# Optimization experiments

Hardware: AMD Instinct MI355X
Metric: run time of the kernel (lower is better)

## Reference

```python
import jax, jax.numpy as jnp
import numpy as np

B, S, D = 8, 2048, 1024


def setup_inputs() -> dict:
    key = jax.random.key(0)
    ks = jax.random.split(key, 9)
    s = 1.0 / np.sqrt(D)
    return {
        "x": jax.random.normal(ks[0], (B, S, D), dtype=jnp.float32),
        "Wq": jax.random.normal(ks[1], (D, D), dtype=jnp.float32) * s,
        "bq": jnp.zeros((D,), dtype=jnp.float32),
        "Wk": jax.random.normal(ks[2], (D, D), dtype=jnp.float32) * s,
        "bk": jnp.zeros((D,), dtype=jnp.float32),
        "Wv": jax.random.normal(ks[3], (D, D), dtype=jnp.float32) * s,
        "bv": jnp.zeros((D,), dtype=jnp.float32),
        "Wo": jax.random.normal(ks[4], (D, D), dtype=jnp.float32) * s,
        "bo": jnp.zeros((D,), dtype=jnp.float32),
    }


def reference(x, Wq, bq, Wk, bk, Wv, bv, Wo, bo):
    # Single-head self-attention with full NxN scores (as in the torch module).
    q = jnp.einsum("bsd,de->bse", x, Wq) + bq
    k = jnp.einsum("bsd,de->bse", x, Wk) + bk
    v = jnp.einsum("bsd,de->bse", x, Wv) + bv
    scores = jnp.einsum("bqd,bkd->bqk", q, k) / jnp.sqrt(jnp.float32(D))
    attn = jax.nn.softmax(scores, axis=-1)
    y = jnp.einsum("bqk,bkd->bqd", attn, v)
    return jnp.einsum("bsd,de->bse", y, Wo) + bo
```

## Files before the change

### kernel.cpp

```cpp
#include <hip/hip_runtime.h>
#include <stdint.h>


using u16 = unsigned short;
using u32 = unsigned int;
using short8  = __attribute__((ext_vector_type(8))) short;
using floatx4 = __attribute__((ext_vector_type(4))) float;

#define GPTR(p) ((__attribute__((address_space(1))) u32*)(p))
#define LPTR(p) ((__attribute__((address_space(3))) u32*)(p))

__device__ __forceinline__ void async_cp16(const void* g, void* l) {
  __builtin_amdgcn_global_load_lds(GPTR(g), LPTR(l), 16, 0, 0);
}

__device__ __forceinline__ u16 f2bf(float f) {
  u32 u = __builtin_bit_cast(u32, f);
  u = (u + 0x7fffu + ((u >> 16) & 1u)) >> 16;
  return (u16)u;
}
__device__ __forceinline__ float bf2f(u16 h) {
  u32 u = ((u32)h) << 16;
  return __builtin_bit_cast(float, u);
}

__device__ __forceinline__ void swz(int gx, int gy, int& bx, int& by) {
  int s = blockIdx.x + gx * blockIdx.y;
  int q = s >> 3;
  by = (s & 7) * (gy >> 3) + q / gx;
  bx = q % gx;
}

__device__ __forceinline__ void gemm_core(
    const u16* __restrict__ A, const u16* __restrict__ B,
    int lda, int ldb, int K, u16* lA, u16* lB, floatx4 acc[4][4])
{
  const int tid  = threadIdx.x;
  const int lane = tid & 63;
  const int w    = tid >> 6;
  const int r8   = lane >> 3;
  const int cg   = (lane & 7) ^ r8;
  const int frow = lane & 15;
  const int fq   = lane >> 4;
  const int wrow = (w >> 1) * 64;
  const int wcol = (w & 1) * 64;

  const u16* gaL = A + (size_t)(w * 32 + r8) * lda + cg * 8;
  const u16* gbL = B + (size_t)(w * 32 + r8) * ldb + cg * 8;
  u16* lAw = lA + (w * 32) * 64;
  u16* lBw = lB + (w * 32) * 64;
  const int x0 = ((0 + fq) ^ (frow & 7)) * 8;
  const int x1 = ((4 + fq) ^ (frow & 7)) * 8;

  for (int k0 = 0; k0 < K; k0 += 64) {
    const u16* ga = gaL + k0;
    const u16* gb = gbL + k0;
#pragma unroll
    for (int t = 0; t < 4; ++t) {
      async_cp16(ga + (size_t)(t * 8) * lda, lAw + t * 8 * 64);
      async_cp16(gb + (size_t)(t * 8) * ldb, lBw + t * 8 * 64);
    }
    __syncthreads();

#pragma unroll
    for (int sub = 0; sub < 2; ++sub) {
      const int xs = sub ? x1 : x0;
      short8 af[4], bfr[4];
#pragma unroll
      for (int i = 0; i < 4; ++i)
        af[i] = *(const short8*)(lA + (wrow + i * 16 + frow) * 64 + xs);
#pragma unroll
      for (int j = 0; j < 4; ++j)
        bfr[j] = *(const short8*)(lB + (wcol + j * 16 + frow) * 64 + xs);
#pragma unroll
      for (int i = 0; i < 4; ++i)
#pragma unroll
        for (int j = 0; j < 4; ++j)
          acc[i][j] = __builtin_amdgcn_mfma_f32_16x16x32_bf16(af[i], bfr[j], acc[i][j], 0, 0, 0);
    }
    __syncthreads();
  }
}

__global__ __launch_bounds__(256) void k_cast_x(const float* __restrict__ x, u16* __restrict__ xb) {
  size_t i = ((size_t)blockIdx.x * 256 + threadIdx.x) * 8;
  float4 a = *(const float4*)(x + i);
  float4 b = *(const float4*)(x + i + 4);
  u16 o[8] __attribute__((aligned(16)));
  o[0] = f2bf(a.x); o[1] = f2bf(a.y); o[2] = f2bf(a.z); o[3] = f2bf(a.w);
  o[4] = f2bf(b.x); o[5] = f2bf(b.y); o[6] = f2bf(b.z); o[7] = f2bf(b.w);
  *(uint4*)(xb + i) = *(const uint4*)o;
}

__global__ __launch_bounds__(256) void k_cast_wt(
    const float* __restrict__ Wq, const float* __restrict__ Wk,
    const float* __restrict__ Wo, const float* __restrict__ Wv,
    u16* __restrict__ WT, u16* __restrict__ Wvb)
{
  __shared__ float t[32][33];
  const int z = blockIdx.z;
  const int c = threadIdx.x & 31, r = threadIdx.x >> 5;
  if (z == 3) {
#pragma unroll
    for (int p = 0; p < 4; ++p) {
      const size_t idx = (size_t)(blockIdx.y * 32 + r + 8 * p) * 1024 + blockIdx.x * 32 + c;
      Wvb[idx] = f2bf(Wv[idx]);
    }
    return;
  }
  const float* W = (z == 0) ? Wq : (z == 1) ? Wk : Wo;
  u16* out = WT + (size_t)z * 1024 * 1024;
#pragma unroll
  for (int p = 0; p < 4; ++p)
    t[r + 8 * p][c] = W[(size_t)(blockIdx.y * 32 + r + 8 * p) * 1024 + blockIdx.x * 32 + c];
  __syncthreads();
#pragma unroll
  for (int p = 0; p < 4; ++p)
    out[(size_t)(blockIdx.x * 32 + r + 8 * p) * 1024 + blockIdx.y * 32 + c] = f2bf(t[c][r + 8 * p]);
}

__global__ __launch_bounds__(256) void k_bvo(
    const float* __restrict__ bv, const float* __restrict__ Wo, float* __restrict__ bvo)
{
  const int nb = blockIdx.x & 3, jc = blockIdx.x >> 2;
  const int n = nb * 256 + threadIdx.x;
  float s = 0.f;
#pragma unroll 4
  for (int j = jc * 64; j < jc * 64 + 64; ++j) s += bv[j] * Wo[(size_t)j * 1024 + n];
  atomicAdd(&bvo[n], s);
}

__global__ __launch_bounds__(256, 4) void k_wvo_part(
    const u16* __restrict__ WoT, const u16* __restrict__ Wvb, float* __restrict__ Pf)
{
  __shared__ u16 lA[8192], lB[8192];
  const int bx = blockIdx.x, by = blockIdx.y, z = blockIdx.z;
  const u16* Am = WoT + (size_t)by * 128 * 1024 + z * 256;
  const u16* Bm = Wvb + (size_t)bx * 128 * 1024 + z * 256;
  floatx4 acc[4][4] = {};
  gemm_core(Am, Bm, 1024, 1024, 256, lA, lB, acc);

  float* out = Pf + (size_t)z * 1024 * 1024;
  const int lane = threadIdx.x & 63, w = threadIdx.x >> 6;
  const int wrow = (w >> 1) * 64, wcol = (w & 1) * 64;
#pragma unroll
  for (int j = 0; j < 4; ++j) {
    const int c = bx * 128 + wcol + j * 16 + (lane & 15);
#pragma unroll
    for (int i = 0; i < 4; ++i) {
      const int m0 = by * 128 + wrow + i * 16 + (lane >> 4) * 4;
#pragma unroll
      for (int r = 0; r < 4; ++r)
        out[(size_t)(m0 + r) * 1024 + c] = acc[i][j][r];
    }
  }
}

__global__ __launch_bounds__(256) void k_wvo_red(
    const float* __restrict__ Pf, u16* __restrict__ WvoT)
{
  const size_t e = ((size_t)blockIdx.x * 256 + threadIdx.x) * 8;
  u16 o[8] __attribute__((aligned(16)));
#pragma unroll
  for (int h = 0; h < 2; ++h) {
    float4 s = *(const float4*)(Pf + e + h * 4);
#pragma unroll
    for (int z = 1; z < 4; ++z) {
      float4 p = *(const float4*)(Pf + (size_t)z * 1024 * 1024 + e + h * 4);
      s.x += p.x; s.y += p.y; s.z += p.z; s.w += p.w;
    }
    o[h * 4 + 0] = f2bf(s.x); o[h * 4 + 1] = f2bf(s.y);
    o[h * 4 + 2] = f2bf(s.z); o[h * 4 + 3] = f2bf(s.w);
  }
  *(uint4*)(WvoT + e) = *(const uint4*)o;
}

__global__ __launch_bounds__(256, 4) void k_qkv(
    const u16* __restrict__ XB, const u16* __restrict__ WT,
    const float* __restrict__ bq, const float* __restrict__ bk, const float* __restrict__ bvo,
    u16* __restrict__ Q, u16* __restrict__ Kb, u16* __restrict__ Vt)
{
  __shared__ u16 smem[17408];
  u16* lA = smem;
  u16* lB = smem + 8192;
  int bx, by; swz(8, 128, bx, by);
  const int mode = blockIdx.z;
  const u16* Am = XB + (size_t)by * 128 * 1024;
  const int ws_idx = (mode == 2) ? 3 : mode;
  const u16* Bm = WT + (size_t)ws_idx * 1024 * 1024 + (size_t)bx * 128 * 1024;
  const float* bias = (mode == 0) ? bq : (mode == 1) ? bk : bvo;
  floatx4 acc[4][4] = {};
  gemm_core(Am, Bm, 1024, 1024, 1024, lA, lB, acc);

  const int tid = threadIdx.x, lane = tid & 63, w = tid >> 6;
  const int lane15 = lane & 15, fq = lane >> 4;
  const int wrow = (w >> 1) * 64, wcol = (w & 1) * 64;

  if (mode == 2) {
    u16* T = smem;
    __syncthreads();
#pragma unroll
    for (int j = 0; j < 4; ++j) {
      const int c = wcol + j * 16 + lane15;
      const float bb = bias[bx * 128 + c];
#pragma unroll
      for (int i = 0; i < 4; ++i)
#pragma unroll
        for (int r = 0; r < 4; ++r)
          T[c * 136 + wrow + i * 16 + fq * 4 + r] = f2bf(acc[i][j][r] + bb);
    }
    __syncthreads();
    const int b = by >> 4, s0 = (by & 15) * 128, c0 = bx * 128;
#pragma unroll
    for (int kk = 0; kk < 8; ++kk) {
      const int cr = (tid >> 4) + 16 * kk, pos = tid & 15;
      uint4 val = *(const uint4*)(T + cr * 136 + pos * 8);
      *(uint4*)(Vt + ((size_t)(b * 1024 + c0 + cr)) * 2048 + s0 + pos * 8) = val;
    }
    return;
  }

#pragma unroll
  for (int j = 0; j < 4; ++j) {
    const int c = bx * 128 + wcol + j * 16 + lane15;
    const float bb = bias[c];
#pragma unroll
    for (int i = 0; i < 4; ++i) {
      const int m0 = by * 128 + wrow + i * 16 + fq * 4;
#pragma unroll
      for (int r = 0; r < 4; ++r) {
        const float v = acc[i][j][r] + bb;
        if (mode == 0) Q[(size_t)(m0 + r) * 1024 + c] = f2bf(v * 0.03125f);
        else           Kb[(size_t)(m0 + r) * 1024 + c] = f2bf(v);
      }
    }
  }
}

__global__ __launch_bounds__(256, 4) void k_scores(
    const u16* __restrict__ Q, const u16* __restrict__ Kb, u16* __restrict__ P,
    float* __restrict__ rowsum)
{
  __shared__ u16 lA[8192], lB[8192];
  const int id = blockIdx.x;
  const int b = id & 7, rest = id >> 3;
  const int bx = rest & 15, by = rest >> 4;
  const u16* Am = Q  + (size_t)b * 2048 * 1024 + (size_t)by * 128 * 1024;
  const u16* Bm = Kb + (size_t)b * 2048 * 1024 + (size_t)bx * 128 * 1024;
  floatx4 acc[4][4] = {};
  gemm_core(Am, Bm, 1024, 1024, 1024, lA, lB, acc);

  u16* Pb = P + (size_t)b * 2048 * 2048;
  const int lane = threadIdx.x & 63, w = threadIdx.x >> 6;
  const int lane15 = lane & 15, fq = lane >> 4;
  const int wrow = (w >> 1) * 64, wcol = (w & 1) * 64;
#pragma unroll
  for (int i = 0; i < 4; ++i) {
#pragma unroll
    for (int r = 0; r < 4; ++r) {
      const int m = by * 128 + wrow + i * 16 + fq * 4 + r;
      float part = 0.f;
#pragma unroll
      for (int j = 0; j < 4; ++j) {
        const int c = bx * 128 + wcol + j * 16 + lane15;
        const float e = __expf(acc[i][j][r]);
        const u16 h = f2bf(e);
        Pb[(size_t)m * 2048 + c] = h;
        part += bf2f(h);
      }
      part += __shfl_xor(part, 1, 64);
      part += __shfl_xor(part, 2, 64);
      part += __shfl_xor(part, 4, 64);
      part += __shfl_xor(part, 8, 64);
      if (lane15 == 0) atomicAdd(&rowsum[b * 2048 + m], part);
    }
  }
}

__global__ __launch_bounds__(256, 4) void k_pv_out(
    const u16* __restrict__ P, const u16* __restrict__ Vt,
    const float* __restrict__ bo, const float* __restrict__ rowsum,
    float* __restrict__ out)
{
  __shared__ u16 lA[8192], lB[8192];
  const int id = blockIdx.x;
  const int b = id & 7, rest = id >> 3;
  const int bx = rest & 7, by = rest >> 3;
  const u16* Am = P  + (size_t)b * 2048 * 2048 + (size_t)by * 128 * 2048;
  const u16* Bm = Vt + (size_t)b * 1024 * 2048 + (size_t)bx * 128 * 2048;
  floatx4 acc[4][4] = {};
  gemm_core(Am, Bm, 2048, 2048, 2048, lA, lB, acc);

  float* outb = out + (size_t)b * 2048 * 1024;
  const int lane = threadIdx.x & 63, w = threadIdx.x >> 6;
  const int lane15 = lane & 15, fq = lane >> 4;
  const int wrow = (w >> 1) * 64, wcol = (w & 1) * 64;
  float bb[4];
#pragma unroll
  for (int j = 0; j < 4; ++j) bb[j] = bo[bx * 128 + wcol + j * 16 + lane15];
#pragma unroll
  for (int i = 0; i < 4; ++i) {
#pragma unroll
    for (int r = 0; r < 4; ++r) {
      const int m = by * 128 + wrow + i * 16 + fq * 4 + r;
      const float inv = 1.0f / rowsum[b * 2048 + m];
#pragma unroll
      for (int j = 0; j < 4; ++j) {
        const int c = bx * 128 + wcol + j * 16 + lane15;
        outb[(size_t)m * 1024 + c] = acc[i][j][r] * inv + bb[j];
      }
    }
  }
}

extern "C" void kernel_launch(void* const* d_in, const int* in_sizes, int n_in,
                              void* d_out, int out_size, void* d_ws, size_t ws_size,
                              hipStream_t stream) {
  const float* x  = (const float*)d_in[0];
  const float* Wq = (const float*)d_in[1];
  const float* bq = (const float*)d_in[2];
  const float* Wk = (const float*)d_in[3];
  const float* bk = (const float*)d_in[4];
  const float* Wv = (const float*)d_in[5];
  const float* bv = (const float*)d_in[6];
  const float* Wo = (const float*)d_in[7];
  const float* bo = (const float*)d_in[8];
  float* out = (float*)d_out;

  char* ws = (char*)d_ws;
  u16* XB  = (u16*)(ws + 0);
  u16* WT  = (u16*)(ws + 33554432);
  u16* Q   = (u16*)(ws + 41943040);
  u16* Kb  = (u16*)(ws + 75497472);
  u16* Vt  = (u16*)(ws + 109051904);
  u16* P   = (u16*)(ws + 142606336);
  u16* Wvb = Kb;
  float* bvo    = (float*)P;
  float* WvoPf  = (float*)(ws + 142606336 + 4194304);
  float* rowsum = (float*)XB;

  if (ws_size < 209715200) return;

  k_cast_wt  <<<dim3(32, 32, 4), 256, 0, stream>>>(Wq, Wk, Wo, Wv, WT, Wvb);
  k_cast_x   <<<8192, 256, 0, stream>>>(x, XB);
  hipMemsetAsync(bvo, 0, 1024 * sizeof(float), stream);
  k_bvo      <<<64, 256, 0, stream>>>(bv, Wo, bvo);
  k_wvo_part <<<dim3(8, 8, 4), 256, 0, stream>>>(WT + (size_t)2 * 1024 * 1024, Wvb, WvoPf);
  k_wvo_red  <<<512, 256, 0, stream>>>(WvoPf, WT + (size_t)3 * 1024 * 1024);
  k_qkv      <<<dim3(8, 128, 3), 256, 0, stream>>>(XB, WT, bq, bk, bvo, Q, Kb, Vt);
  hipMemsetAsync(rowsum, 0, 16384 * sizeof(float), stream);
  k_scores   <<<2048, 256, 0, stream>>>(Q, Kb, P, rowsum);
  k_pv_out   <<<1024, 256, 0, stream>>>(P, Vt, bo, rowsum, out);
}
```

Baseline: 419.4 us.

## Use double-buffered 256x256 tile GEMM with 512 threads for QKV, scores and PV

Adds a new GEMM core that computes 256x256 output tiles with 8 waves. It double-buffers K-slices in 128KB of dynamic LDS using async global-to-LDS copies and explicit vmcnt waits, and raises wave priority around the MFMA bursts. The QKV, scores and PV kernels move onto this core, with grids resized to match. The V transpose epilogue now goes through a per-wave swizzled scratch instead of a block-wide barrier. The aim is better operand reuse and load/compute overlap. The cost is one block per CU because of the LDS size, a heavier register footprint, and very few blocks for the PV kernel.

New measurement: 427.8 us. 1.02x slower.

```diff
diff --git a/kernel.cpp b/kernel.cpp
--- a/kernel.cpp
+++ b/kernel.cpp
@@ -9,6 +9,7 @@
 
 #define GPTR(p) ((__attribute__((address_space(1))) u32*)(p))
 #define LPTR(p) ((__attribute__((address_space(3))) u32*)(p))
+#define MFMA16 __builtin_amdgcn_mfma_f32_16x16x32_bf16
 
 __device__ __forceinline__ void async_cp16(const void* g, void* l) {
   __builtin_amdgcn_global_load_lds(GPTR(g), LPTR(l), 16, 0, 0);
@@ -76,9 +77,113 @@
       for (int i = 0; i < 4; ++i)
 #pragma unroll
         for (int j = 0; j < 4; ++j)
-          acc[i][j] = __builtin_amdgcn_mfma_f32_16x16x32_bf16(af[i], bfr[j], acc[i][j], 0, 0, 0);
+          acc[i][j] = MFMA16(af[i], bfr[j], acc[i][j], 0, 0, 0);
     }
     __syncthreads();
+  }
+}
+
+__device__ __forceinline__ void gemm256(
+    const u16* __restrict__ A, const u16* __restrict__ B,
+    int lda, int ldb, int K, u16* smem, floatx4 acc[8][4])
+{
+  const int tid  = threadIdx.x;
+  const int lane = tid & 63;
+  const int w    = tid >> 6;
+  const int frow = lane & 15;
+  const int fq   = lane >> 4;
+  const int wrow = (w >> 2) * 128;
+  const int wcol = (w & 3) * 64;
+  const int x0 = ((0 + fq) ^ (frow & 7)) * 8;
+  const int x1 = ((4 + fq) ^ (frow & 7)) * 8;
+  const int sr = tid >> 3, sl = tid & 7;
+  const size_t aoff = (size_t)sr * lda + ((sl ^ (sr & 7)) << 3);
+  const size_t boff = (size_t)sr * ldb + ((sl ^ (sr & 7)) << 3);
+  const int nt = K >> 6;
+
+  auto stage = [&](int t, int bsel) {
+    const u16* ga = A + t * 64 + aoff;
+    const u16* gb = B + t * 64 + boff;
+    u16* la = smem + bsel * 16384 + tid * 8;
+    u16* lb = smem + 32768 + bsel * 16384 + tid * 8;
+#pragma unroll
+    for (int q = 0; q < 4; ++q)
+      async_cp16(ga + (size_t)(q * 64) * lda, la + q * 4096);
+#pragma unroll
+    for (int q = 0; q < 4; ++q)
+      async_cp16(gb + (size_t)(q * 64) * ldb, lb + q * 4096);
+  };
+
+  stage(0, 0);
+  if (nt > 1) stage(1, 1);
+
+  for (int t = 0; t < nt; ++t) {
+    const u16* la = smem + (t & 1) * 16384;
+    const u16* lb = smem + 32768 + (t & 1) * 16384;
+    if (t + 1 < nt) { asm volatile("s_waitcnt vmcnt(8)" ::: "memory"); }
+    else            { asm volatile("s_waitcnt vmcnt(0)" ::: "memory"); }
+    __builtin_amdgcn_s_barrier();
+
+    short8 af[4][2], b0[2][2], b1[2][2];
+#pragma unroll
+    for (int i = 0; i < 4; ++i) {
+      af[i][0] = *(const short8*)(la + (wrow + i * 16 + frow) * 64 + x0);
+      af[i][1] = *(const short8*)(la + (wrow + i * 16 + frow) * 64 + x1);
+    }
+#pragma unroll
+    for (int j = 0; j < 2; ++j) {
+      b0[j][0] = *(const short8*)(lb + (wcol + j * 16 + frow) * 64 + x0);
+      b0[j][1] = *(const short8*)(lb + (wcol + j * 16 + frow) * 64 + x1);
+    }
+    __builtin_amdgcn_s_setprio(1);
+#pragma unroll
+    for (int i = 0; i < 4; ++i)
+#pragma unroll
+      for (int j = 0; j < 2; ++j) {
+        acc[i][j] = MFMA16(af[i][0], b0[j][0], acc[i][j], 0, 0, 0);
+        acc[i][j] = MFMA16(af[i][1], b0[j][1], acc[i][j], 0, 0, 0);
+      }
+    __builtin_amdgcn_s_setprio(0);
+#pragma unroll
+    for (int j = 0; j < 2; ++j) {
+      b1[j][0] = *(const short8*)(lb + (wcol + (2 + j) * 16 + frow) * 64 + x0);
+      b1[j][1] = *(const short8*)(lb + (wcol + (2 + j) * 16 + frow) * 64 + x1);
+    }
+    __builtin_amdgcn_s_setprio(1);
+#pragma unroll
+    for (int i = 0; i < 4; ++i)
+#pragma unroll
+      for (int j = 0; j < 2; ++j) {
+        acc[i][2 + j] = MFMA16(af[i][0], b1[j][0], acc[i][2 + j], 0, 0, 0);
+        acc[i][2 + j] = MFMA16(af[i][1], b1[j][1], acc[i][2 + j], 0, 0, 0);
+      }
+    __builtin_amdgcn_s_setprio(0);
+#pragma unroll
+    for (int i = 0; i < 4; ++i) {
+      af[i][0] = *(const short8*)(la + (wrow + (4 + i) * 16 + frow) * 64 + x0);
+      af[i][1] = *(const short8*)(la + (wrow + (4 + i) * 16 + frow) * 64 + x1);
+    }
+    __builtin_amdgcn_s_setprio(1);
+#pragma unroll
+    for (int i = 0; i < 4; ++i)
+#pragma unroll
+      for (int j = 0; j < 2; ++j) {
+        acc[4 + i][2 + j] = MFMA16(af[i][0], b1[j][0], acc[4 + i][2 + j], 0, 0, 0);
+        acc[4 + i][2 + j] = MFMA16(af[i][1], b1[j][1], acc[4 + i][2 + j], 0, 0, 0);
+      }
+    __builtin_amdgcn_s_setprio(0);
+    __builtin_amdgcn_s_setprio(1);
+#pragma unroll
+    for (int i = 0; i < 4; ++i)
+#pragma unroll
+      for (int j = 0; j < 2; ++j) {
+        acc[4 + i][j] = MFMA16(af[i][0], b0[j][0], acc[4 + i][j], 0, 0, 0);
+        acc[4 + i][j] = MFMA16(af[i][1], b0[j][1], acc[4 + i][j], 0, 0, 0);
+      }
+    __builtin_amdgcn_s_setprio(0);
+
+    __builtin_amdgcn_s_barrier();
+    if (t + 2 < nt) stage(t + 2, t & 1);
   }
 }
 
@@ -175,58 +280,58 @@
   *(uint4*)(WvoT + e) = *(const uint4*)o;
 }
 
-__global__ __launch_bounds__(256, 4) void k_qkv(
+__global__ __launch_bounds__(512, 2) void k_qkv2(
     const u16* __restrict__ XB, const u16* __restrict__ WT,
     const float* __restrict__ bq, const float* __restrict__ bk, const float* __restrict__ bvo,
     u16* __restrict__ Q, u16* __restrict__ Kb, u16* __restrict__ Vt)
 {
-  __shared__ u16 smem[17408];
-  u16* lA = smem;
-  u16* lB = smem + 8192;
-  int bx, by; swz(8, 128, bx, by);
+  extern __shared__ __align__(16) u16 smem[];
+  int bx, by; swz(4, 64, bx, by);
   const int mode = blockIdx.z;
-  const u16* Am = XB + (size_t)by * 128 * 1024;
+  const u16* Am = XB + (size_t)by * 256 * 1024;
   const int ws_idx = (mode == 2) ? 3 : mode;
-  const u16* Bm = WT + (size_t)ws_idx * 1024 * 1024 + (size_t)bx * 128 * 1024;
+  const u16* Bm = WT + (size_t)ws_idx * 1024 * 1024 + (size_t)bx * 256 * 1024;
   const float* bias = (mode == 0) ? bq : (mode == 1) ? bk : bvo;
-  floatx4 acc[4][4] = {};
-  gemm_core(Am, Bm, 1024, 1024, 1024, lA, lB, acc);
+  floatx4 acc[8][4] = {};
+  gemm256(Am, Bm, 1024, 1024, 1024, smem, acc);
 
   const int tid = threadIdx.x, lane = tid & 63, w = tid >> 6;
-  const int lane15 = lane & 15, fq = lane >> 4;
-  const int wrow = (w >> 1) * 64, wcol = (w & 1) * 64;
+  const int frow = lane & 15, fq = lane >> 4;
+  const int wrow = (w >> 2) * 128, wcol = (w & 3) * 64;
 
   if (mode == 2) {
-    u16* T = smem;
-    __syncthreads();
+    u16* scr = smem + w * 8192;
 #pragma unroll
     for (int j = 0; j < 4; ++j) {
-      const int c = wcol + j * 16 + lane15;
-      const float bb = bias[bx * 128 + c];
-#pragma unroll
-      for (int i = 0; i < 4; ++i)
-#pragma unroll
-        for (int r = 0; r < 4; ++r)
-          T[c * 136 + wrow + i * 16 + fq * 4 + r] = f2bf(acc[i][j][r] + bb);
-    }
-    __syncthreads();
-    const int b = by >> 4, s0 = (by & 15) * 128, c0 = bx * 128;
-#pragma unroll
-    for (int kk = 0; kk < 8; ++kk) {
-      const int cr = (tid >> 4) + 16 * kk, pos = tid & 15;
-      uint4 val = *(const uint4*)(T + cr * 136 + pos * 8);
-      *(uint4*)(Vt + ((size_t)(b * 1024 + c0 + cr)) * 2048 + s0 + pos * 8) = val;
+      const int dl = j * 16 + frow;
+      const float bb = bias[bx * 256 + wcol + dl];
+#pragma unroll
+      for (int i = 0; i < 8; ++i) {
+        const int sl_ = i * 16 + fq * 4;
+        const u32 lo = (u32)f2bf(acc[i][j][0]  + bb) | ((u32)f2bf(acc[i][j][1] + bb) << 16);
+        const u32 hi = (u32)f2bf(acc[i][j][2]  + bb) | ((u32)f2bf(acc[i][j][3] + bb) << 16);
+        u32* p = (u32*)(scr + dl * 128 + (((sl_ >> 3) ^ (dl & 15)) << 3) + (sl_ & 7));
+        p[0] = lo; p[1] = hi;
+      }
+    }
+    const int b = by >> 3, s0 = (by & 7) * 256;
+    const int dq = lane >> 4, cc = lane & 15;
+#pragma unroll
+    for (int it = 0; it < 16; ++it) {
+      const int dl = it * 4 + dq;
+      uint4 v = *(const uint4*)(scr + dl * 128 + ((cc ^ (dl & 15)) << 3));
+      *(uint4*)(Vt + ((size_t)(b * 1024 + bx * 256 + wcol + dl)) * 2048 + s0 + wrow + cc * 8) = v;
     }
     return;
   }
 
 #pragma unroll
   for (int j = 0; j < 4; ++j) {
-    const int c = bx * 128 + wcol + j * 16 + lane15;
+    const int c = bx * 256 + wcol + j * 16 + frow;
     const float bb = bias[c];
 #pragma unroll
-    for (int i = 0; i < 4; ++i) {
-      const int m0 = by * 128 + wrow + i * 16 + fq * 4;
+    for (int i = 0; i < 8; ++i) {
+      const int m0 = by * 256 + wrow + i * 16 + fq * 4;
 #pragma unroll
       for (int r = 0; r < 4; ++r) {
         const float v = acc[i][j][r] + bb;
@@ -237,32 +342,32 @@
   }
 }
 
-__global__ __launch_bounds__(256, 4) void k_scores(
+__global__ __launch_bounds__(512, 2) void k_scores2(
     const u16* __restrict__ Q, const u16* __restrict__ Kb, u16* __restrict__ P,
     float* __restrict__ rowsum)
 {
-  __shared__ u16 lA[8192], lB[8192];
+  extern __shared__ __align__(16) u16 smem[];
   const int id = blockIdx.x;
   const int b = id & 7, rest = id >> 3;
-  const int bx = rest & 15, by = rest >> 4;
-  const u16* Am = Q  + (size_t)b * 2048 * 1024 + (size_t)by * 128 * 1024;
-  const u16* Bm = Kb + (size_t)b * 2048 * 1024 + (size_t)bx * 128 * 1024;
-  floatx4 acc[4][4] = {};
-  gemm_core(Am, Bm, 1024, 1024, 1024, lA, lB, acc);
+  const int bx = rest & 7, by = rest >> 3;
+  const u16* Am = Q  + (size_t)b * 2048 * 1024 + (size_t)by * 256 * 1024;
+  const u16* Bm = Kb + (size_t)b * 2048 * 1024 + (size_t)bx * 256 * 1024;
+  floatx4 acc[8][4] = {};
+  gemm256(Am, Bm, 1024, 1024, 1024, smem, acc);
 
   u16* Pb = P + (size_t)b * 2048 * 2048;
   const int lane = threadIdx.x & 63, w = threadIdx.x >> 6;
-  const int lane15 = lane & 15, fq = lane >> 4;
-  const int wrow = (w >> 1) * 64, wcol = (w & 1) * 64;
-#pragma unroll
-  for (int i = 0; i < 4; ++i) {
+  const int frow = lane & 15, fq = lane >> 4;
+  const int wrow = (w >> 2) * 128, wcol = (w & 3) * 64;
+#pragma unroll
+  for (int i = 0; i < 8; ++i) {
 #pragma unroll
     for (int r = 0; r < 4; ++r) {
-      const int m = by * 128 + wrow + i * 16 + fq * 4 + r;
+      const int m = by * 256 + wrow + i * 16 + fq * 4 + r;
       float part = 0.f;
 #pragma unroll
       for (int j = 0; j < 4; ++j) {
-        const int c = bx * 128 + wcol + j * 16 + lane15;
+        const int c = bx * 256 + wcol + j * 16 + frow;
         const float e = __expf(acc[i][j][r]);
         const u16 h = f2bf(e);
         Pb[(size_t)m * 2048 + c] = h;
@@ -272,41 +377,41 @@
       part += __shfl_xor(part, 2, 64);
       part += __shfl_xor(part, 4, 64);
       part += __shfl_xor(part, 8, 64);
-      if (lane15 == 0) atomicAdd(&rowsum[b * 2048 + m], part);
-    }
-  }
-}
-
-__global__ __launch_bounds__(256, 4) void k_pv_out(
+      if (frow == 0) atomicAdd(&rowsum[b * 2048 + m], part);
+    }
+  }
+}
+
+__global__ __launch_bounds__(512, 2) void k_pv2(
     const u16* __restrict__ P, const u16* __restrict__ Vt,
     const float* __restrict__ bo, const float* __restrict__ rowsum,
     float* __restrict__ out)
 {
-  __shared__ u16 lA[8192], lB[8192];
+  extern __shared__ __align__(16) u16 smem[];
   const int id = blockIdx.x;
   const int b = id & 7, rest = id >> 3;
-  const int bx = rest & 7, by = rest >> 3;
-  const u16* Am = P  + (size_t)b * 2048 * 2048 + (size_t)by * 128 * 2048;
-  const u16* Bm = Vt + (size_t)b * 1024 * 2048 + (size_t)bx * 128 * 2048;
-  floatx4 acc[4][4] = {};
-  gemm_core(Am, Bm, 2048, 2048, 2048, lA, lB, acc);
+  const int bx = rest & 3, by = rest >> 2;
+  const u16* Am = P  + (size_t)b * 2048 * 2048 + (size_t)by * 256 * 2048;
+  const u16* Bm = Vt + (size_t)b * 1024 * 2048 + (size_t)bx * 256 * 2048;
+  floatx4 acc[8][4] = {};
+  gemm256(Am, Bm, 2048, 2048, 2048, smem, acc);
 
   float* outb = out + (size_t)b * 2048 * 1024;
   const int lane = threadIdx.x & 63, w = threadIdx.x >> 6;
-  const int lane15 = lane & 15, fq = lane >> 4;
-  const int wrow = (w >> 1) * 64, wcol = (w & 1) * 64;
+  const int frow = lane & 15, fq = lane >> 4;
+  const int wrow = (w >> 2) * 128, wcol = (w & 3) * 64;
   float bb[4];
 #pragma unroll
-  for (int j = 0; j < 4; ++j) bb[j] = bo[bx * 128 + wcol + j * 16 + lane15];
-#pragma unroll
-  for (int i = 0; i < 4; ++i) {
+  for (int j = 0; j < 4; ++j) bb[j] = bo[bx * 256 + wcol + j * 16 + frow];
+#pragma unroll
+  for (int i = 0; i < 8; ++i) {
 #pragma unroll
     for (int r = 0; r < 4; ++r) {
-      const int m = by * 128 + wrow + i * 16 + fq * 4 + r;
+      const int m = by * 256 + wrow + i * 16 + fq * 4 + r;
       const float inv = 1.0f / rowsum[b * 2048 + m];
 #pragma unroll
       for (int j = 0; j < 4; ++j) {
-        const int c = bx * 128 + wcol + j * 16 + lane15;
+        const int c = bx * 256 + wcol + j * 16 + frow;
         outb[(size_t)m * 1024 + c] = acc[i][j][r] * inv + bb[j];
       }
     }
@@ -341,14 +446,25 @@
 
   if (ws_size < 209715200) return;
 
+  static int attr_set = 0;
+  if (!attr_set) {
+    hipFuncSetAttribute(reinterpret_cast<const void*>(k_qkv2),
+                        hipFuncAttributeMaxDynamicSharedMemorySize, 131072);
+    hipFuncSetAttribute(reinterpret_cast<const void*>(k_scores2),
+                        hipFuncAttributeMaxDynamicSharedMemorySize, 131072);
+    hipFuncSetAttribute(reinterpret_cast<const void*>(k_pv2),
+                        hipFuncAttributeMaxDynamicSharedMemorySize, 131072);
+    attr_set = 1;
+  }
+
   k_cast_wt  <<<dim3(32, 32, 4), 256, 0, stream>>>(Wq, Wk, Wo, Wv, WT, Wvb);
   k_cast_x   <<<8192, 256, 0, stream>>>(x, XB);
   hipMemsetAsync(bvo, 0, 1024 * sizeof(float), stream);
   k_bvo      <<<64, 256, 0, stream>>>(bv, Wo, bvo);
   k_wvo_part <<<dim3(8, 8, 4), 256, 0, stream>>>(WT + (size_t)2 * 1024 * 1024, Wvb, WvoPf);
   k_wvo_red  <<<512, 256, 0, stream>>>(WvoPf, WT + (size_t)3 * 1024 * 1024);
-  k_qkv      <<<dim3(8, 128, 3), 256, 0, stream>>>(XB, WT, bq, bk, bvo, Q, Kb, Vt);
+  k_qkv2     <<<dim3(4, 64, 3), 512, 131072, stream>>>(XB, WT, bq, bk, bvo, Q, Kb, Vt);
   hipMemsetAsync(rowsum, 0, 16384 * sizeof(float), stream);
-  k_scores   <<<2048, 256, 0, stream>>>(Q, Kb, P, rowsum);
-  k_pv_out   <<<1024, 256, 0, stream>>>(P, Vt, bo, rowsum, out);
-}
+  k_scores2  <<<512, 512, 131072, stream>>>(Q, Kb, P, rowsum);
+  k_pv2      <<<256, 512, 131072, stream>>>(P, Vt, bo, rowsum, out);
+}
```
